# Kernel tuning notes

Measured on AMD Instinct MI355X. Metric: run time of the kernel, lower is better.

Reference implementation:

```python
import jax, jax.numpy as jnp
import numpy as np

NUM_ITERATIONS = 5
M_CHECKS, N_CODE, ROW_WEIGHT = 63, 127, 8
BATCH = 4096
BIG = 1e10  # sentinel used by optimized_topk for masked-out entries


def _make_H():
    # Deterministic sparse parity-check matrix with fixed row weight.
    rng = np.random.default_rng(0)
    H = np.zeros((M_CHECKS, N_CODE), dtype=np.int32)
    for i in range(M_CHECKS):
        H[i, rng.choice(N_CODE, ROW_WEIGHT, replace=False)] = 1
    return H


def setup_inputs() -> dict:
    key = jax.random.key(0)
    k1, k2 = jax.random.split(key)
    soft_input = jax.random.normal(k1, (BATCH, N_CODE), dtype=jnp.float32)
    labels = jax.random.randint(k2, (BATCH, N_CODE), 0, 2, dtype=jnp.int32)
    H = jnp.asarray(_make_H())
    normalizor = jnp.full((1,), -2.5, dtype=jnp.float32)  # decoder_check_normalizor
    return {"soft_input": soft_input, "labels": labels, "H": H,
            "normalizor": normalizor}


def _nms_iteration(cur, Hf, supp, norm):
    # variable -> check messages: (B, m, n)
    vc = cur[:, None, :] * Hf
    # sign part: product of signs over each check row, extrinsic per edge
    signs = jnp.sign(supp + vc)  # supplement makes masked entries sign +1
    total_sign = jnp.prod(signs, axis=2, keepdims=True) * Hf
    result_sign = total_sign * signs
    # magnitude part: extrinsic min via top-2 smallest magnitudes per row
    av = jnp.abs(vc)
    proc = jnp.where(av * Hf == 0.0, BIG, av * Hf)
    top2 = -jax.lax.top_k(-proc, 2)[0]           # (B, m, 2) two smallest
    smallest = top2[..., 0:1]
    second = top2[..., 1:2]
    updated = jnp.where(av == smallest, second, smallest) * Hf
    # normalized min-sum check -> variable messages
    cv = norm * updated * jax.lax.stop_gradient(result_sign)
    # marginalize: posterior = prior + sum of incoming check messages
    return cur + jnp.sum(cv, axis=1)


def reference(soft_input, labels, H, normalizor):
    Hf = H.astype(jnp.float32)                # (m, n)
    supp = (1.0 - Hf)[None]                   # supplement_matrix, (1, m, n)
    norm = jax.nn.softplus(normalizor)        # softplus(decoder_check_normalizor)
    outs = [soft_input]
    cur = soft_input
    for _ in range(NUM_ITERATIONS):
        cur = _nms_iteration(cur, Hf, supp, norm)
        outs.append(cur)
    return jnp.stack(outs, axis=0), labels    # (iters+1, B, n), (B, n)
```

## Files before the change

kernel.cpp:

```cpp
#include <hip/hip_runtime.h>
#include <math.h>

#define M_CHECKS 63
#define N_CODE   127
#define ROW_W    8
#define BATCH    4096
#define NITER    5
#define BIGF     1e10f
#define MAXDEG   16

__launch_bounds__(256, 4)
__global__ void nms_decode(const float* __restrict__ soft,
                           const int*   __restrict__ labels,
                           const int*   __restrict__ H,
                           const float* __restrict__ normalizor,
                           float*       __restrict__ out) {
    __shared__ float  cur[4][128];
    __shared__ int    sidx[M_CHECKS * ROW_W];
    __shared__ float4 chk[4][64];
    __shared__ int    csc[N_CODE * MAXDEG];
    __shared__ int    cnt[128];

    const int tid  = threadIdx.x;
    const int w    = tid >> 6;
    const int lane = tid & 63;
    const int row  = blockIdx.x * 4 + w;

    if (tid < 128) cnt[tid] = 0;

    {
        const unsigned long long below =
            (lane == 0) ? 0ull : ((~0ull) >> (64 - lane));
        for (int i = w; i < M_CHECKS; i += 4) {
            const int c0 = lane;
            const int c1 = lane + 64;
            const int b0 = (H[i * N_CODE + c0] != 0) ? 1 : 0;
            const int b1 = (c1 < N_CODE) ? ((H[i * N_CODE + c1] != 0) ? 1 : 0) : 0;
            unsigned long long m0 = __ballot(b0);
            unsigned long long m1 = __ballot(b1);
            if (b0) {
                int pos = __popcll(m0 & below);
                if (pos < ROW_W) sidx[i * ROW_W + pos] = c0;
            }
            if (b1) {
                int pos = __popcll(m0) + __popcll(m1 & below);
                if (pos < ROW_W) sidx[i * ROW_W + pos] = c1;
            }
        }
    }
    __syncthreads();

    if (w == 0 && lane < M_CHECKS) {
        #pragma unroll
        for (int p = 0; p < ROW_W; ++p) {
            int c = sidx[lane * ROW_W + p];
            int slot = atomicAdd(&cnt[c], 1);
            if (slot < MAXDEG) csc[c * MAXDEG + slot] = lane;
        }
    }
    __syncthreads();

    const float norm = log1pf(expf(normalizor[0]));
    float* outLabels = out + (size_t)(NITER + 1) * BATCH * N_CODE;

    const int j0 = lane;
    const int j1 = lane + 64;
    float x0, x1 = 0.0f;
    {
        const size_t base = (size_t)row * N_CODE;
        x0 = soft[base + j0];
        cur[w][j0] = x0;
        out[base + j0] = x0;
        outLabels[base + j0] = (float)labels[base + j0];
        if (lane < 63) {
            x1 = soft[base + j1];
            cur[w][j1] = x1;
            out[base + j1] = x1;
            outLabels[base + j1] = (float)labels[base + j1];
        }
    }
    const int deg0 = min(cnt[j0], MAXDEG);
    const int deg1 = (lane < 63) ? min(cnt[j1], MAXDEG) : 0;

    asm volatile("s_waitcnt lgkmcnt(0)" ::: "memory");
    __builtin_amdgcn_sched_barrier(0);

    for (int it = 0; it < NITER; ++it) {
        if (lane < M_CHECKS) {
            float m1 = BIGF, m2 = BIGF, sprod = 1.0f;
            #pragma unroll
            for (int p = 0; p < ROW_W; ++p) {
                int c   = sidx[lane * ROW_W + p];
                float x = cur[w][c];
                float s = (x > 0.0f) ? 1.0f : ((x < 0.0f) ? -1.0f : 0.0f);
                sprod *= s;
                float av   = fabsf(x);
                float proc = (av == 0.0f) ? BIGF : av;
                if (proc < m1) { m2 = m1; m1 = proc; }
                else if (proc < m2) { m2 = proc; }
            }
            chk[w][lane] = make_float4(m1, m2, sprod, 0.0f);
        }
        asm volatile("s_waitcnt lgkmcnt(0)" ::: "memory");
        __builtin_amdgcn_sched_barrier(0);

        {
            float av0 = fabsf(x0);
            float s0  = (x0 > 0.0f) ? 1.0f : ((x0 < 0.0f) ? -1.0f : 0.0f);
            float acc0 = 0.0f;
            for (int e = 0; e < deg0; ++e) {
                int i = csc[j0 * MAXDEG + e];
                float4 c4 = chk[w][i];
                float upd = (av0 == c4.x) ? c4.y : c4.x;
                acc0 += upd * c4.z;
            }
            x0 += norm * s0 * acc0;

            float av1 = fabsf(x1);
            float s1  = (x1 > 0.0f) ? 1.0f : ((x1 < 0.0f) ? -1.0f : 0.0f);
            float acc1 = 0.0f;
            for (int e = 0; e < deg1; ++e) {
                int i = csc[j1 * MAXDEG + e];
                float4 c4 = chk[w][i];
                float upd = (av1 == c4.x) ? c4.y : c4.x;
                acc1 += upd * c4.z;
            }
            x1 += norm * s1 * acc1;
        }

        cur[w][j0] = x0;
        if (lane < 63) cur[w][j1] = x1;

        const size_t obase = (size_t)(it + 1) * BATCH * N_CODE + (size_t)row * N_CODE;
        out[obase + j0] = x0;
        if (lane < 63) out[obase + j1] = x1;

        asm volatile("s_waitcnt lgkmcnt(0)" ::: "memory");
        __builtin_amdgcn_sched_barrier(0);
    }
}

extern "C" void kernel_launch(void* const* d_in, const int* in_sizes, int n_in,
                              void* d_out, int out_size, void* d_ws, size_t ws_size,
                              hipStream_t stream) {
    const float* soft       = (const float*)d_in[0];
    const int*   labels     = (const int*)d_in[1];
    const int*   H          = (const int*)d_in[2];
    const float* normalizor = (const float*)d_in[3];
    float*       out        = (float*)d_out;

    nms_decode<<<BATCH / 4, 256, 0, stream>>>(soft, labels, H, normalizor, out);
}
```

Measured before the change: 97.92 us.

## Scatter per-edge check messages into dense slot arrays, replacing CSC gather

Check-node threads now compute each edge's final message (normalized, sign-adjusted extrinsic min) and write it into a zero-initialized per-warp [slot][column] shared buffer. Variable nodes then sum a fixed 16 slots with unrolled, coalesced reads instead of looping over a variable-degree CSC list with indirect float4 gathers. This removes divergent variable-length loops and the indirect loads, at the cost of 32KB more LDS, fixed 16-slot reads, and an upfront zeroing pass. It also drops the MAXDEG clamp on slots, so any column with degree above 16 would write out of bounds.

```diff
diff --git a/kernel.cpp b/kernel.cpp
--- a/kernel.cpp
+++ b/kernel.cpp
@@ -7,7 +7,7 @@
 #define BATCH    4096
 #define NITER    5
 #define BIGF     1e10f
-#define MAXDEG   16
+#define MAXD     16
 
 __launch_bounds__(256, 4)
 __global__ void nms_decode(const float* __restrict__ soft,
@@ -15,18 +15,24 @@
                            const int*   __restrict__ H,
                            const float* __restrict__ normalizor,
                            float*       __restrict__ out) {
-    __shared__ float  cur[4][128];
-    __shared__ int    sidx[M_CHECKS * ROW_W];
-    __shared__ float4 chk[4][64];
-    __shared__ int    csc[N_CODE * MAXDEG];
-    __shared__ int    cnt[128];
+    __shared__ float cur[4][128];
+    __shared__ float cvals[4][MAXD][128];
+    __shared__ int   sidx[M_CHECKS * ROW_W];
+    __shared__ int   sslot[M_CHECKS * ROW_W];
+    __shared__ int   cnt[128];
 
     const int tid  = threadIdx.x;
     const int w    = tid >> 6;
     const int lane = tid & 63;
     const int row  = blockIdx.x * 4 + w;
 
-    if (tid < 128) cnt[tid] = 0;
+    {
+        float4* cv4 = (float4*)cvals;
+        #pragma unroll
+        for (int t = 0; t < (4 * MAXD * 128) / 4 / 256; ++t)
+            cv4[tid + t * 256] = make_float4(0.f, 0.f, 0.f, 0.f);
+        if (tid < 128) cnt[tid] = 0;
+    }
 
     {
         const unsigned long long below =
@@ -54,14 +60,24 @@
         #pragma unroll
         for (int p = 0; p < ROW_W; ++p) {
             int c = sidx[lane * ROW_W + p];
-            int slot = atomicAdd(&cnt[c], 1);
-            if (slot < MAXDEG) csc[c * MAXDEG + slot] = lane;
+            sslot[lane * ROW_W + p] = atomicAdd(&cnt[c], 1);
         }
     }
     __syncthreads();
 
     const float norm = log1pf(expf(normalizor[0]));
     float* outLabels = out + (size_t)(NITER + 1) * BATCH * N_CODE;
+    float* const cvw = &cvals[w][0][0];
+
+    int ec[ROW_W];
+    int widx[ROW_W];
+    if (lane < M_CHECKS) {
+        #pragma unroll
+        for (int p = 0; p < ROW_W; ++p) {
+            ec[p]   = sidx[lane * ROW_W + p];
+            widx[p] = sslot[lane * ROW_W + p] * 128 + ec[p];
+        }
+    }
 
     const int j0 = lane;
     const int j1 = lane + 64;
@@ -79,19 +95,19 @@
             outLabels[base + j1] = (float)labels[base + j1];
         }
     }
-    const int deg0 = min(cnt[j0], MAXDEG);
-    const int deg1 = (lane < 63) ? min(cnt[j1], MAXDEG) : 0;
-
     asm volatile("s_waitcnt lgkmcnt(0)" ::: "memory");
     __builtin_amdgcn_sched_barrier(0);
 
     for (int it = 0; it < NITER; ++it) {
         if (lane < M_CHECKS) {
+            float v[ROW_W];
+            #pragma unroll
+            for (int p = 0; p < ROW_W; ++p) v[p] = cur[w][ec[p]];
+
             float m1 = BIGF, m2 = BIGF, sprod = 1.0f;
             #pragma unroll
             for (int p = 0; p < ROW_W; ++p) {
-                int c   = sidx[lane * ROW_W + p];
-                float x = cur[w][c];
+                float x = v[p];
                 float s = (x > 0.0f) ? 1.0f : ((x < 0.0f) ? -1.0f : 0.0f);
                 sprod *= s;
                 float av   = fabsf(x);
@@ -99,34 +115,26 @@
                 if (proc < m1) { m2 = m1; m1 = proc; }
                 else if (proc < m2) { m2 = proc; }
             }
-            chk[w][lane] = make_float4(m1, m2, sprod, 0.0f);
+            const float nsp = norm * sprod;
+            #pragma unroll
+            for (int p = 0; p < ROW_W; ++p) {
+                float x   = v[p];
+                float s   = (x > 0.0f) ? 1.0f : ((x < 0.0f) ? -1.0f : 0.0f);
+                float av  = fabsf(x);
+                float upd = (av == m1) ? m2 : m1;
+                cvw[widx[p]] = nsp * upd * s;
+            }
         }
         asm volatile("s_waitcnt lgkmcnt(0)" ::: "memory");
         __builtin_amdgcn_sched_barrier(0);
 
-        {
-            float av0 = fabsf(x0);
-            float s0  = (x0 > 0.0f) ? 1.0f : ((x0 < 0.0f) ? -1.0f : 0.0f);
-            float acc0 = 0.0f;
-            for (int e = 0; e < deg0; ++e) {
-                int i = csc[j0 * MAXDEG + e];
-                float4 c4 = chk[w][i];
-                float upd = (av0 == c4.x) ? c4.y : c4.x;
-                acc0 += upd * c4.z;
-            }
-            x0 += norm * s0 * acc0;
-
-            float av1 = fabsf(x1);
-            float s1  = (x1 > 0.0f) ? 1.0f : ((x1 < 0.0f) ? -1.0f : 0.0f);
-            float acc1 = 0.0f;
-            for (int e = 0; e < deg1; ++e) {
-                int i = csc[j1 * MAXDEG + e];
-                float4 c4 = chk[w][i];
-                float upd = (av1 == c4.x) ? c4.y : c4.x;
-                acc1 += upd * c4.z;
-            }
-            x1 += norm * s1 * acc1;
-        }
+        float acc0 = 0.0f, acc1 = 0.0f;
+        #pragma unroll
+        for (int e = 0; e < MAXD; ++e) acc0 += cvw[e * 128 + j0];
+        #pragma unroll
+        for (int e = 0; e < MAXD; ++e) acc1 += cvw[e * 128 + j1];
+        x0 += acc0;
+        x1 += acc1;
 
         cur[w][j0] = x0;
         if (lane < 63) cur[w][j1] = x1;
```

After: 80.27 us. 18.0% less time.
